# Optimization experiments

Hardware: AMD Instinct MI355X
Metric: run time of the kernel (lower is better)

Reference implementation:

```python
import jax, jax.numpy as jnp
import numpy as np

N_HEAD = 16
N_EMBD = 1024
SEQ = 2048
BATCH = 4


def setup_inputs() -> dict:
    key = jax.random.key(0)
    ks = jax.random.split(key, 5)
    s_in = 1.0 / np.sqrt(N_EMBD)
    return {
        "x": jax.random.normal(ks[0], (BATCH, SEQ, N_EMBD), dtype=jnp.float32),
        "W_attn": jax.random.normal(ks[1], (N_EMBD, 3 * N_EMBD), dtype=jnp.float32) * s_in,
        "b_attn": jax.random.normal(ks[2], (3 * N_EMBD,), dtype=jnp.float32) * 0.01,
        "W_proj": jax.random.normal(ks[3], (N_EMBD, N_EMBD), dtype=jnp.float32) * s_in,
        "b_proj": jax.random.normal(ks[4], (N_EMBD,), dtype=jnp.float32) * 0.01,
    }


def reference(x, W_attn, b_attn, W_proj, b_proj):
    B, T, C = x.shape
    H = N_HEAD
    D = C // H  # head dim
    qkv = x @ W_attn + b_attn                      # [B,T,3C]
    q, k, v = jnp.split(qkv, 3, axis=-1)
    # [B,T,C] -> [B,H,T,D]
    q = q.reshape(B, T, H, D).transpose(0, 2, 1, 3)
    k = k.reshape(B, T, H, D).transpose(0, 2, 1, 3)
    v = v.reshape(B, T, H, D).transpose(0, 2, 1, 3)
    scale = 1.0 / np.sqrt(D).astype(np.float32)
    att = jnp.einsum('bhqd,bhkd->bhqk', q, k) * scale   # [B,H,T,T]
    causal = jnp.tril(jnp.ones((T, T), dtype=bool))
    att = jnp.where(causal, att, jnp.finfo(att.dtype).min)
    att = jax.nn.softmax(att, axis=-1)
    y = jnp.einsum('bhqk,bhkd->bhqd', att, v)            # [B,H,T,D]
    y = y.transpose(0, 2, 1, 3).reshape(B, T, C)
    return y @ W_proj + b_proj
```

## Files before the change

### kernel.cpp

```cpp
#include <hip/hip_runtime.h>
#include <stdint.h>

typedef __attribute__((ext_vector_type(8))) short short8;
typedef __attribute__((ext_vector_type(4))) short short4v;
typedef __attribute__((ext_vector_type(4))) float f32x4;
typedef __attribute__((ext_vector_type(2))) unsigned int uint2v;

#define B_ 4
#define T_ 2048
#define C_ 1024
#define H_ 16
#define D_ 64
#define C3_ 3072

#define AS1 __attribute__((address_space(1)))
#define AS3 __attribute__((address_space(3)))

#define QK_SCALE 0.18033688f

__device__ __forceinline__ unsigned short f2bf(float f) {
    union { float f; uint32_t u; } v; v.f = f;
    uint32_t r = v.u + 0x7FFFu + ((v.u >> 16) & 1u);
    return (unsigned short)(r >> 16);
}

__device__ __forceinline__ uint32_t pk_bf16(float lo, float hi) {
    uint32_t r;
    asm("v_cvt_pk_bf16_f32 %0, %1, %2" : "=v"(r) : "v"(lo), "v"(hi));
    return r;
}

__global__ void k_cvt_bf16(const float* __restrict__ in, unsigned short* __restrict__ out, int n4) {
    int i = blockIdx.x * blockDim.x + threadIdx.x;
    if (i >= n4) return;
    float4 v = ((const float4*)in)[i];
    unsigned short o0 = f2bf(v.x), o1 = f2bf(v.y), o2 = f2bf(v.z), o3 = f2bf(v.w);
    unsigned long long packed = (unsigned long long)o0 | ((unsigned long long)o1 << 16)
        | ((unsigned long long)o2 << 32) | ((unsigned long long)o3 << 48);
    *(unsigned long long*)(out + (size_t)i * 4) = packed;
}

__global__ void k_wtrans(const float* __restrict__ W, unsigned short* __restrict__ WT, int K, int N) {
    __shared__ float t[32][33];
    int n0 = blockIdx.x * 32, k0 = blockIdx.y * 32;
    int tx = threadIdx.x, ty = threadIdx.y;
#pragma unroll
    for (int i = 0; i < 4; ++i)
        t[ty + i * 8][tx] = W[(size_t)(k0 + ty + i * 8) * N + n0 + tx];
    __syncthreads();
#pragma unroll
    for (int i = 0; i < 4; ++i)
        WT[(size_t)(n0 + ty + i * 8) * K + k0 + tx] = f2bf(t[tx][ty + i * 8]);
}

__global__ void k_prep_vt(const unsigned short* __restrict__ qkv, unsigned short* __restrict__ vt) {
    int bh = blockIdx.y; int b = bh >> 4, h = bh & 15;
    int t0 = blockIdx.x * 64;
    __shared__ unsigned short tile[64][72];
    int tid = threadIdx.x;
    int r = tid >> 3;
    int c = (tid & 7) * 8;
#pragma unroll
    for (int rr = 0; rr < 64; rr += 32) {
        const unsigned short* src = qkv + (size_t)(b * T_ + t0 + r + rr) * C3_ + 2 * C_ + h * D_ + c;
        short8 v = *(const short8*)src;
#pragma unroll
        for (int j = 0; j < 8; ++j) tile[r + rr][c + j] = (unsigned short)v[j];
    }
    __syncthreads();
#pragma unroll
    for (int rr = 0; rr < 64; rr += 32) {
        int d = r + rr;
        short8 sv;
#pragma unroll
        for (int j = 0; j < 8; ++j) sv[j] = (short)tile[c + j][d];
        *(short8*)(vt + (size_t)bh * D_ * T_ + (size_t)d * T_ + t0 + c) = sv;
    }
}

template<bool OUT_BF16>
__global__ __launch_bounds__(256, 2) void k_gemm_bt(const unsigned short* __restrict__ A,
                                                    const unsigned short* __restrict__ BT,
                                                    const float* __restrict__ bias,
                                                    unsigned short* __restrict__ outb,
                                                    float* __restrict__ outf,
                                                    int M, int N, int K) {
    __shared__ __align__(16) char arena[73728];
    int tid = threadIdx.x;
    int w = tid >> 6, lane = tid & 63;
    int wrow = w >> 1, wcol = w & 1;

    int lin = blockIdx.y * gridDim.x + blockIdx.x;
    int nwg8 = (gridDim.x * gridDim.y) >> 3;
    int newlin = (lin & 7) * nwg8 + (lin >> 3);
    int bx = newlin % gridDim.x;
    int by = newlin / gridDim.x;
    int m0 = by * 256, n0 = bx * 128;

    int lr = lane & 15, lg = lane >> 4;

    f32x4 acc[8][4] = {};

    int scb = ((tid & 3) << 4) ^ (((tid >> 3) & 3) << 4);
    int grow = tid >> 2;
    const char* sA[4];
    const char* sB[2];
#pragma unroll
    for (int rr = 0; rr < 4; ++rr)
        sA[rr] = (const char*)A + (size_t)(m0 + grow + rr * 64) * K * 2 + scb;
#pragma unroll
    for (int rr = 0; rr < 2; ++rr)
        sB[rr] = (const char*)BT + (size_t)(n0 + grow + rr * 64) * K * 2 + scb;

    int inner = (lg * 16) ^ (((lr >> 1) & 3) << 4);
    int aoff = wrow * 8192 + lr * 64 + inner;
    int boff = 16384 + wcol * 4096 + lr * 64 + inner;

#define GSTAGE(OFS)                                                                                 \
    {                                                                                               \
        _Pragma("unroll")                                                                           \
        for (int rr = 0; rr < 4; ++rr) {                                                            \
            __builtin_amdgcn_global_load_lds((const AS1 void*)sA[rr],                               \
                (AS3 void*)(arena + (OFS) + tid * 16 + rr * 4096), 16, 0, 0);                       \
            sA[rr] += 64;                                                                           \
        }                                                                                           \
        _Pragma("unroll")                                                                           \
        for (int rr = 0; rr < 2; ++rr) {                                                            \
            __builtin_amdgcn_global_load_lds((const AS1 void*)sB[rr],                               \
                (AS3 void*)(arena + (OFS) + 16384 + tid * 16 + rr * 4096), 16, 0, 0);               \
            sB[rr] += 64;                                                                           \
        }                                                                                           \
    }

#define GCOMPUTE(OFS)                                                                               \
    {                                                                                               \
        short8 af[8], bf[4];                                                                        \
        _Pragma("unroll")                                                                           \
        for (int i = 0; i < 8; ++i)                                                                 \
            af[i] = *(const short8*)(arena + (OFS) + aoff + i * 1024);                              \
        _Pragma("unroll")                                                                           \
        for (int j = 0; j < 4; ++j)                                                                 \
            bf[j] = *(const short8*)(arena + (OFS) + boff + j * 1024);                              \
        __builtin_amdgcn_s_setprio(1);                                                              \
        _Pragma("unroll")                                                                           \
        for (int i = 0; i < 8; ++i)                                                                 \
            _Pragma("unroll")                                                                       \
            for (int j = 0; j < 4; ++j)                                                             \
                acc[i][j] = __builtin_amdgcn_mfma_f32_16x16x32_bf16(af[i], bf[j], acc[i][j], 0, 0, 0); \
        __builtin_amdgcn_s_setprio(0);                                                              \
    }

    int NT = K >> 5;
    int ofs0 = 0, ofs1 = 24576, ofs2 = 49152;

    GSTAGE(ofs0);
    GSTAGE(ofs1);
    asm volatile("s_waitcnt vmcnt(6)" ::: "memory");
    __builtin_amdgcn_s_barrier();
    __builtin_amdgcn_sched_barrier(0);

    for (int t = 0; t < NT; ++t) {
        bool pf = (t + 2 < NT);
        if (pf) GSTAGE(ofs2);
        GCOMPUTE(ofs0);
        if (pf) { asm volatile("s_waitcnt vmcnt(6)" ::: "memory"); }
        else    { asm volatile("s_waitcnt vmcnt(0)" ::: "memory"); }
        __builtin_amdgcn_s_barrier();
        __builtin_amdgcn_sched_barrier(0);
        int tmp = ofs0; ofs0 = ofs1; ofs1 = ofs2; ofs2 = tmp;
    }
#undef GSTAGE
#undef GCOMPUTE

#pragma unroll
    for (int i = 0; i < 8; ++i) {
        int row = m0 + wrow * 128 + i * 16 + lg * 4;
#pragma unroll
        for (int j = 0; j < 4; ++j) {
            int col = n0 + wcol * 64 + j * 16 + lr;
            float bv = bias[col];
#pragma unroll
            for (int r = 0; r < 4; ++r) {
                float v = acc[i][j][r] + bv;
                if (OUT_BF16) {
                    if (col < C_) v *= QK_SCALE;
                    outb[(size_t)(row + r) * N + col] = f2bf(v);
                } else {
                    outf[(size_t)(row + r) * N + col] = v;
                }
            }
        }
    }
}

__global__ __launch_bounds__(256, 3) void k_gemm_bt128(const unsigned short* __restrict__ A,
                                                       const unsigned short* __restrict__ BT,
                                                       const float* __restrict__ bias,
                                                       float* __restrict__ outf,
                                                       int M, int N, int K) {
    __shared__ __align__(16) char arena[49152];
    int tid = threadIdx.x;
    int w = tid >> 6, lane = tid & 63;
    int wrow = w >> 1, wcol = w & 1;

    int lin = blockIdx.y * gridDim.x + blockIdx.x;
    int nwg8 = (gridDim.x * gridDim.y) >> 3;
    int newlin = (lin & 7) * nwg8 + (lin >> 3);
    int bx = newlin % gridDim.x;
    int by = newlin / gridDim.x;
    int m0 = by * 128, n0 = bx * 128;

    int lr = lane & 15, lg = lane >> 4;

    f32x4 acc[4][4] = {};

    int scb = ((tid & 3) << 4) ^ (((tid >> 3) & 3) << 4);
    int grow = tid >> 2;
    const char* sA[2];
    const char* sB[2];
#pragma unroll
    for (int rr = 0; rr < 2; ++rr) {
        sA[rr] = (const char*)A + (size_t)(m0 + grow + rr * 64) * K * 2 + scb;
        sB[rr] = (const char*)BT + (size_t)(n0 + grow + rr * 64) * K * 2 + scb;
    }

    int inner = (lg * 16) ^ (((lr >> 1) & 3) << 4);
    int aoff = wrow * 4096 + lr * 64 + inner;
    int boff = 8192 + wcol * 4096 + lr * 64 + inner;

#define GSTAGE(OFS)                                                                                 \
    {                                                                                               \
        _Pragma("unroll")                                                                           \
        for (int rr = 0; rr < 2; ++rr) {                                                            \
            __builtin_amdgcn_global_load_lds((const AS1 void*)sA[rr],                               \
                (AS3 void*)(arena + (OFS) + tid * 16 + rr * 4096), 16, 0, 0);                       \
            sA[rr] += 64;                                                                           \
            __builtin_amdgcn_global_load_lds((const AS1 void*)sB[rr],                               \
                (AS3 void*)(arena + (OFS) + 8192 + tid * 16 + rr * 4096), 16, 0, 0);                \
            sB[rr] += 64;                                                                           \
        }                                                                                           \
    }

#define GCOMPUTE(OFS)                                                                               \
    {                                                                                               \
        short8 af[4], bf[4];                                                                        \
        _Pragma("unroll")                                                                           \
        for (int i = 0; i < 4; ++i)                                                                 \
            af[i] = *(const short8*)(arena + (OFS) + aoff + i * 1024);                              \
        _Pragma("unroll")                                                                           \
        for (int j = 0; j < 4; ++j)                                                                 \
            bf[j] = *(const short8*)(arena + (OFS) + boff + j * 1024);                              \
        __builtin_amdgcn_s_setprio(1);                                                              \
        _Pragma("unroll")                                                                           \
        for (int i = 0; i < 4; ++i)                                                                 \
            _Pragma("unroll")                                                                       \
            for (int j = 0; j < 4; ++j)                                                             \
                acc[i][j] = __builtin_amdgcn_mfma_f32_16x16x32_bf16(af[i], bf[j], acc[i][j], 0, 0, 0); \
        __builtin_amdgcn_s_setprio(0);                                                              \
    }

    int NT = K >> 5;
    int ofs0 = 0, ofs1 = 16384, ofs2 = 32768;

    GSTAGE(ofs0);
    GSTAGE(ofs1);
    asm volatile("s_waitcnt vmcnt(4)" ::: "memory");
    __builtin_amdgcn_s_barrier();
    __builtin_amdgcn_sched_barrier(0);

    for (int t = 0; t < NT; ++t) {
        bool pf = (t + 2 < NT);
        if (pf) GSTAGE(ofs2);
        GCOMPUTE(ofs0);
        if (pf) { asm volatile("s_waitcnt vmcnt(4)" ::: "memory"); }
        else    { asm volatile("s_waitcnt vmcnt(0)" ::: "memory"); }
        __builtin_amdgcn_s_barrier();
        __builtin_amdgcn_sched_barrier(0);
        int tmp = ofs0; ofs0 = ofs1; ofs1 = ofs2; ofs2 = tmp;
    }
#undef GSTAGE
#undef GCOMPUTE

#pragma unroll
    for (int i = 0; i < 4; ++i) {
        int row = m0 + wrow * 64 + i * 16 + lg * 4;
#pragma unroll
        for (int j = 0; j < 4; ++j) {
            int col = n0 + wcol * 64 + j * 16 + lr;
            float bv = bias[col];
#pragma unroll
            for (int r = 0; r < 4; ++r)
                outf[(size_t)(row + r) * N + col] = acc[i][j][r] + bv;
        }
    }
}

__global__ __launch_bounds__(256, 4) void k_attn(const unsigned short* __restrict__ qkv,
                                                 const unsigned short* __restrict__ vt,
                                                 unsigned short* __restrict__ y) {
    __shared__ __align__(16) char arena[40960];
    int tid = threadIdx.x;
    int w = tid >> 6, lane = tid & 63;
    int lr = lane & 15, lg = lane >> 4;

    int bid = blockIdx.x;
    int bid2 = (bid & 7) * 128 + (bid >> 3);
    int bh = bid2 >> 4, pair = bid2 & 15;
    int b = bh >> 4, h = bh & 15;

    const unsigned short* kbase = qkv + (size_t)(b * T_) * C3_ + C_ + h * D_;
    const unsigned short* vtb = vt + (size_t)bh * D_ * T_;

    int sw_ = (lr & 7) << 4;
    int RB0 = lr * 128 + ((lg * 16) ^ sw_);
    int RB1 = RB0 ^ 64;
    int jl = (lr >> 1) & 3;
    int pbase = 32768 + w * 2048 + lr * 128
              + ((((lg >> 1) ^ (lr & 1)) << 4) | (((lg & 1) ^ (lr >> 3)) << 3));
    int pwa[4];
#pragma unroll
    for (int j = 0; j < 4; ++j) pwa[j] = pbase + ((j ^ jl) << 5);
    int prd0 = 32768 + w * 2048 + lr * 128 + ((lg ^ (lr & 7)) << 4);
    int prd1 = prd0 ^ 64;
    int hs = lr & 8;
    int prA0a = prd0 + hs,       prA0b = prd0 + (8 ^ hs);
    int prA1a = prd1 + hs,       prA1b = prd1 + (8 ^ hs);

    int row0 = tid >> 3, row1 = 32 + (tid >> 3);
    int scol0 = ((tid & 7) << 4) ^ ((row0 & 7) << 4);
    int scol1 = ((tid & 7) << 4) ^ ((row1 & 7) << 4);

    const char *sK0, *sK1, *sV0, *sV1;

#define ASTAGE(LDSOFF)                                                                                  \
    {                                                                                                   \
        __builtin_amdgcn_global_load_lds((const AS1 void*)sK0, (AS3 void*)(arena + (LDSOFF) + w * 1024), 16, 0, 0);          \
        __builtin_amdgcn_global_load_lds((const AS1 void*)sK1, (AS3 void*)(arena + (LDSOFF) + 4096 + w * 1024), 16, 0, 0);   \
        __builtin_amdgcn_global_load_lds((const AS1 void*)sV0, (AS3 void*)(arena + 16384 + (LDSOFF) + w * 1024), 16, 0, 0);  \
        __builtin_amdgcn_global_load_lds((const AS1 void*)sV1, (AS3 void*)(arena + 16384 + (LDSOFF) + 4096 + w * 1024), 16, 0, 0); \
        sK0 += 64 * C3_ * 2; sK1 += 64 * C3_ * 2; sV0 += 128; sV1 += 128;                               \
    }

#define ACOMPUTE(LDSOFF, KT)                                                                            \
    {                                                                                                   \
        f32x4 s[4];                                                                                     \
        __builtin_amdgcn_s_setprio(1);                                                                  \
        _Pragma("unroll")                                                                               \
        for (int j = 0; j < 4; ++j) {                                                                   \
            short8 kf0 = *(const short8*)(arena + RB0 + (LDSOFF) + j * 2048);                           \
            short8 kf1 = *(const short8*)(arena + RB1 + (LDSOFF) + j * 2048);                           \
            f32x4 z = {};                                                                               \
            z = __builtin_amdgcn_mfma_f32_16x16x32_bf16(kf0, qf0, z, 0, 0, 0);                          \
            s[j] = __builtin_amdgcn_mfma_f32_16x16x32_bf16(kf1, qf1, z, 0, 0, 0);                       \
        }                                                                                               \
        __builtin_amdgcn_s_setprio(0);                                                                  \
        if ((KT) == ntiles - 1) {                                                                       \
            int kb = (KT) * 64 + lg * 4 - qv;                                                           \
            _Pragma("unroll")                                                                           \
            for (int j = 0; j < 4; ++j)                                                                 \
                _Pragma("unroll")                                                                       \
                for (int r = 0; r < 4; ++r)                                                             \
                    if (kb + j * 16 + r > 0) s[j][r] = -INFINITY;                                       \
        }                                                                                               \
        _Pragma("unroll")                                                                               \
        for (int j = 0; j < 4; ++j)                                                                     \
            _Pragma("unroll")                                                                           \
            for (int r = 0; r < 4; ++r) {                                                               \
                float pv = __builtin_amdgcn_exp2f(s[j][r]);                                             \
                s[j][r] = pv;                                                                           \
                ls += pv;                                                                               \
            }                                                                                           \
        _Pragma("unroll")                                                                               \
        for (int j = 0; j < 4; ++j) {                                                                   \
            uint2v W;                                                                                   \
            W[0] = pk_bf16(s[j][0], s[j][1]);                                                           \
            W[1] = pk_bf16(s[j][2], s[j][3]);                                                           \
            *(uint2v*)(arena + pwa[j]) = W;                                                             \
        }                                                                                               \
        short4v l0 = *(const short4v*)(arena + prA0a);                                                  \
        short4v h0 = *(const short4v*)(arena + prA0b);                                                  \
        short4v l1 = *(const short4v*)(arena + prA1a);                                                  \
        short4v h1 = *(const short4v*)(arena + prA1b);                                                  \
        short8 pa0 = __builtin_shufflevector(l0, h0, 0, 1, 2, 3, 4, 5, 6, 7);                           \
        short8 pa1 = __builtin_shufflevector(l1, h1, 0, 1, 2, 3, 4, 5, 6, 7);                           \
        __builtin_amdgcn_s_setprio(1);                                                                  \
        _Pragma("unroll")                                                                               \
        for (int dt = 0; dt < 4; ++dt) {                                                                \
            short8 vf0 = *(const short8*)(arena + RB0 + 16384 + (LDSOFF) + dt * 2048);                  \
            short8 vf1 = *(const short8*)(arena + RB1 + 16384 + (LDSOFF) + dt * 2048);                  \
            o[dt] = __builtin_amdgcn_mfma_f32_16x16x32_bf16(pa0, vf0, o[dt], 0, 0, 0);                  \
            o[dt] = __builtin_amdgcn_mfma_f32_16x16x32_bf16(pa1, vf1, o[dt], 0, 0, 0);                  \
        }                                                                                               \
        __builtin_amdgcn_s_setprio(0);                                                                  \
    }

#pragma unroll 1
    for (int half = 0; half < 2; ++half) {
        int qt = half ? (31 - pair) : pair;
        int q0 = qt * 64;
        int ntiles = qt + 1;

        const unsigned short* qrow = qkv + (size_t)(b * T_ + q0 + w * 16 + lr) * C3_ + h * D_;
        short8 qf0 = *(const short8*)(qrow + lg * 8);
        short8 qf1 = *(const short8*)(qrow + 32 + lg * 8);

        f32x4 o[4] = {};
        float ls = 0.f;
        int qv = q0 + w * 16 + lr;

        sK0 = (const char*)(kbase + (size_t)row0 * C3_) + scol0;
        sK1 = (const char*)(kbase + (size_t)row1 * C3_) + scol1;
        sV0 = (const char*)(vtb + (size_t)row0 * T_) + scol0;
        sV1 = (const char*)(vtb + (size_t)row1 * T_) + scol1;

        ASTAGE(0);
        asm volatile("s_waitcnt vmcnt(0)" ::: "memory");
        __syncthreads();

#pragma unroll 1
        for (int kt = 0; kt < ntiles; kt += 2) {
            if (kt + 1 < ntiles) ASTAGE(8192);
            ACOMPUTE(0, kt);
            asm volatile("s_waitcnt vmcnt(0)" ::: "memory");
            __syncthreads();
            if (kt + 1 < ntiles) {
                if (kt + 2 < ntiles) ASTAGE(0);
                ACOMPUTE(8192, kt + 1);
                asm volatile("s_waitcnt vmcnt(0)" ::: "memory");
                __syncthreads();
            }
        }

        ls += __shfl_xor(ls, 16);
        ls += __shfl_xor(ls, 32);
#pragma unroll
        for (int r = 0; r < 4; ++r) {
            float lst = __shfl(ls, lg * 4 + r, 64);
            float inv = 1.0f / lst;
            int q = q0 + w * 16 + lg * 4 + r;
            unsigned short* yrow = y + (size_t)(b * T_ + q) * C_ + h * D_;
#pragma unroll
            for (int dt = 0; dt < 4; ++dt)
                yrow[dt * 16 + lr] = f2bf(o[dt][r] * inv);
        }
    }
#undef ASTAGE
#undef ACOMPUTE
}

extern "C" void kernel_launch(void* const* d_in, const int* in_sizes, int n_in,
                              void* d_out, int out_size, void* d_ws, size_t ws_size,
                              hipStream_t stream) {
    const float* x  = (const float*)d_in[0];
    const float* Wa = (const float*)d_in[1];
    const float* ba = (const float*)d_in[2];
    const float* Wp = (const float*)d_in[3];
    const float* bp = (const float*)d_in[4];
    float* out = (float*)d_out;

    char* ws = (char*)d_ws;
    unsigned short* xb  = (unsigned short*)(ws);
    unsigned short* wat = (unsigned short*)(ws + 16777216);
    unsigned short* wpt = (unsigned short*)(ws + 23068672);
    unsigned short* qkv = (unsigned short*)(ws + 25165824);
    unsigned short* vt  = (unsigned short*)(ws + 75497472);
    unsigned short* y   = xb;

    k_cvt_bf16<<<8192, 256, 0, stream>>>(x, xb, (B_ * T_ * C_) / 4);
    k_wtrans<<<dim3(C3_ / 32, C_ / 32), dim3(32, 8), 0, stream>>>(Wa, wat, C_, C3_);
    k_wtrans<<<dim3(C_ / 32, C_ / 32), dim3(32, 8), 0, stream>>>(Wp, wpt, C_, C_);
    k_gemm_bt<true><<<dim3(C3_ / 128, (B_ * T_) / 256), 256, 0, stream>>>(
        xb, wat, ba, qkv, nullptr, B_ * T_, C3_, C_);
    k_prep_vt<<<dim3(T_ / 64, B_ * H_), 256, 0, stream>>>(qkv, vt);
    k_attn<<<1024, 256, 0, stream>>>(qkv, vt, y);
    k_gemm_bt128<<<dim3(C_ / 128, (B_ * T_) / 128), 256, 0, stream>>>(
        y, wpt, bp, out, B_ * T_, C_, C_);
}
```

Measured before the change: 158.8 us.

## Double attention query tile per block to reuse K/V tiles across two row groups

Each wave in the attention kernel now handles 32 query rows (two 16-row groups) instead of 16, so every block covers a 128-row query tile. Each K/V tile staged into LDS therefore feeds twice as many MFMAs, and half as many blocks are launched. The P scratch area per wave doubles, so LDS grows to 48KB and the launch bound drops to 3 blocks per CU. Register pressure rises and fewer blocks are in flight. Causal masking is now applied over the last two key tiles to cover the larger diagonal.

```diff
diff --git a/kernel.cpp b/kernel.cpp
--- a/kernel.cpp
+++ b/kernel.cpp
@@ -295,17 +295,17 @@
     }
 }
 
-__global__ __launch_bounds__(256, 4) void k_attn(const unsigned short* __restrict__ qkv,
+__global__ __launch_bounds__(256, 3) void k_attn(const unsigned short* __restrict__ qkv,
                                                  const unsigned short* __restrict__ vt,
                                                  unsigned short* __restrict__ y) {
-    __shared__ __align__(16) char arena[40960];
+    __shared__ __align__(16) char arena[49152];
     int tid = threadIdx.x;
     int w = tid >> 6, lane = tid & 63;
     int lr = lane & 15, lg = lane >> 4;
 
     int bid = blockIdx.x;
-    int bid2 = (bid & 7) * 128 + (bid >> 3);
-    int bh = bid2 >> 4, pair = bid2 & 15;
+    int bid2 = (bid & 7) * 64 + (bid >> 3);
+    int bh = bid2 >> 3, pair = bid2 & 7;
     int b = bh >> 4, h = bh & 15;
 
     const unsigned short* kbase = qkv + (size_t)(b * T_) * C3_ + C_ + h * D_;
@@ -314,17 +314,18 @@
     int sw_ = (lr & 7) << 4;
     int RB0 = lr * 128 + ((lg * 16) ^ sw_);
     int RB1 = RB0 ^ 64;
+
     int jl = (lr >> 1) & 3;
-    int pbase = 32768 + w * 2048 + lr * 128
+    int pbase = 32768 + w * 4096 + lr * 128
               + ((((lg >> 1) ^ (lr & 1)) << 4) | (((lg & 1) ^ (lr >> 3)) << 3));
     int pwa[4];
 #pragma unroll
     for (int j = 0; j < 4; ++j) pwa[j] = pbase + ((j ^ jl) << 5);
-    int prd0 = 32768 + w * 2048 + lr * 128 + ((lg ^ (lr & 7)) << 4);
+    int prd0 = 32768 + w * 4096 + lr * 128 + ((lg ^ (lr & 7)) << 4);
     int prd1 = prd0 ^ 64;
     int hs = lr & 8;
-    int prA0a = prd0 + hs,       prA0b = prd0 + (8 ^ hs);
-    int prA1a = prd1 + hs,       prA1b = prd1 + (8 ^ hs);
+    int prA0a = prd0 + hs, prA0b = prd0 + (8 ^ hs);
+    int prA1a = prd1 + hs, prA1b = prd1 + (8 ^ hs);
 
     int row0 = tid >> 3, row1 = 32 + (tid >> 3);
     int scol0 = ((tid & 7) << 4) ^ ((row0 & 7) << 4);
@@ -343,70 +344,89 @@
 
 #define ACOMPUTE(LDSOFF, KT)                                                                            \
     {                                                                                                   \
-        f32x4 s[4];                                                                                     \
+        f32x4 s0[4], s1[4];                                                                             \
         __builtin_amdgcn_s_setprio(1);                                                                  \
         _Pragma("unroll")                                                                               \
         for (int j = 0; j < 4; ++j) {                                                                   \
             short8 kf0 = *(const short8*)(arena + RB0 + (LDSOFF) + j * 2048);                           \
             short8 kf1 = *(const short8*)(arena + RB1 + (LDSOFF) + j * 2048);                           \
-            f32x4 z = {};                                                                               \
-            z = __builtin_amdgcn_mfma_f32_16x16x32_bf16(kf0, qf0, z, 0, 0, 0);                          \
-            s[j] = __builtin_amdgcn_mfma_f32_16x16x32_bf16(kf1, qf1, z, 0, 0, 0);                       \
+            f32x4 z0 = {}, z1 = {};                                                                     \
+            z0 = __builtin_amdgcn_mfma_f32_16x16x32_bf16(kf0, qA0, z0, 0, 0, 0);                        \
+            s0[j] = __builtin_amdgcn_mfma_f32_16x16x32_bf16(kf1, qA1, z0, 0, 0, 0);                     \
+            z1 = __builtin_amdgcn_mfma_f32_16x16x32_bf16(kf0, qB0, z1, 0, 0, 0);                        \
+            s1[j] = __builtin_amdgcn_mfma_f32_16x16x32_bf16(kf1, qB1, z1, 0, 0, 0);                     \
         }                                                                                               \
         __builtin_amdgcn_s_setprio(0);                                                                  \
-        if ((KT) == ntiles - 1) {                                                                       \
-            int kb = (KT) * 64 + lg * 4 - qv;                                                           \
+        if ((KT) >= ntiles - 2) {                                                                       \
+            int kb0 = (KT) * 64 + lg * 4 - qv0;                                                         \
             _Pragma("unroll")                                                                           \
             for (int j = 0; j < 4; ++j)                                                                 \
                 _Pragma("unroll")                                                                       \
-                for (int r = 0; r < 4; ++r)                                                             \
-                    if (kb + j * 16 + r > 0) s[j][r] = -INFINITY;                                       \
+                for (int r = 0; r < 4; ++r) {                                                           \
+                    if (kb0 + j * 16 + r > 0)      s0[j][r] = -INFINITY;                                \
+                    if (kb0 - 16 + j * 16 + r > 0) s1[j][r] = -INFINITY;         \
+                }                                                                                       \
         }                                                                                               \
         _Pragma("unroll")                                                                               \
         for (int j = 0; j < 4; ++j)                                                                     \
             _Pragma("unroll")                                                                           \
             for (int r = 0; r < 4; ++r) {                                                               \
-                float pv = __builtin_amdgcn_exp2f(s[j][r]);                                             \
-                s[j][r] = pv;                                                                           \
-                ls += pv;                                                                               \
+                float p0 = __builtin_amdgcn_exp2f(s0[j][r]);                                            \
+                float p1 = __builtin_amdgcn_exp2f(s1[j][r]);                                            \
+                s0[j][r] = p0; ls0 += p0;                                                               \
+                s1[j][r] = p1; ls1 += p1;                                                               \
             }                                                                                           \
         _Pragma("unroll")                                                                               \
         for (int j = 0; j < 4; ++j) {                                                                   \
-            uint2v W;                                                                                   \
-            W[0] = pk_bf16(s[j][0], s[j][1]);                                                           \
-            W[1] = pk_bf16(s[j][2], s[j][3]);                                                           \
-            *(uint2v*)(arena + pwa[j]) = W;                                                             \
+            uint2v W0, W1;                                                                              \
+            W0[0] = pk_bf16(s0[j][0], s0[j][1]);                                                        \
+            W0[1] = pk_bf16(s0[j][2], s0[j][3]);                                                        \
+            W1[0] = pk_bf16(s1[j][0], s1[j][1]);                                                        \
+            W1[1] = pk_bf16(s1[j][2], s1[j][3]);                                                        \
+            *(uint2v*)(arena + pwa[j]) = W0;                                                            \
+            *(uint2v*)(arena + pwa[j] + 2048) = W1;                                                     \
         }                                                                                               \
-        short4v l0 = *(const short4v*)(arena + prA0a);                                                  \
-        short4v h0 = *(const short4v*)(arena + prA0b);                                                  \
-        short4v l1 = *(const short4v*)(arena + prA1a);                                                  \
-        short4v h1 = *(const short4v*)(arena + prA1b);                                                  \
-        short8 pa0 = __builtin_shufflevector(l0, h0, 0, 1, 2, 3, 4, 5, 6, 7);                           \
-        short8 pa1 = __builtin_shufflevector(l1, h1, 0, 1, 2, 3, 4, 5, 6, 7);                           \
+        short4v l00 = *(const short4v*)(arena + prA0a);                                                 \
+        short4v h00 = *(const short4v*)(arena + prA0b);                                                 \
+        short4v l01 = *(const short4v*)(arena + prA1a);                                                 \
+        short4v h01 = *(const short4v*)(arena + prA1b);                                                 \
+        short4v l10 = *(const short4v*)(arena + prA0a + 2048);                                          \
+        short4v h10 = *(const short4v*)(arena + prA0b + 2048);                                          \
+        short4v l11 = *(const short4v*)(arena + prA1a + 2048);                                          \
+        short4v h11 = *(const short4v*)(arena + prA1b + 2048);                                          \
+        short8 pa00 = __builtin_shufflevector(l00, h00, 0, 1, 2, 3, 4, 5, 6, 7);                        \
+        short8 pa01 = __builtin_shufflevector(l01, h01, 0, 1, 2, 3, 4, 5, 6, 7);                        \
+        short8 pa10 = __builtin_shufflevector(l10, h10, 0, 1, 2, 3, 4, 5, 6, 7);                        \
+        short8 pa11 = __builtin_shufflevector(l11, h11, 0, 1, 2, 3, 4, 5, 6, 7);                        \
         __builtin_amdgcn_s_setprio(1);                                                                  \
         _Pragma("unroll")                                                                               \
         for (int dt = 0; dt < 4; ++dt) {                                                                \
             short8 vf0 = *(const short8*)(arena + RB0 + 16384 + (LDSOFF) + dt * 2048);                  \
             short8 vf1 = *(const short8*)(arena + RB1 + 16384 + (LDSOFF) + dt * 2048);                  \
-            o[dt] = __builtin_amdgcn_mfma_f32_16x16x32_bf16(pa0, vf0, o[dt], 0, 0, 0);                  \
-            o[dt] = __builtin_amdgcn_mfma_f32_16x16x32_bf16(pa1, vf1, o[dt], 0, 0, 0);                  \
+            o0[dt] = __builtin_amdgcn_mfma_f32_16x16x32_bf16(pa00, vf0, o0[dt], 0, 0, 0);               \
+            o0[dt] = __builtin_amdgcn_mfma_f32_16x16x32_bf16(pa01, vf1, o0[dt], 0, 0, 0);               \
+            o1[dt] = __builtin_amdgcn_mfma_f32_16x16x32_bf16(pa10, vf0, o1[dt], 0, 0, 0);               \
+            o1[dt] = __builtin_amdgcn_mfma_f32_16x16x32_bf16(pa11, vf1, o1[dt], 0, 0, 0);               \
         }                                                                                               \
         __builtin_amdgcn_s_setprio(0);                                                                  \
     }
 
 #pragma unroll 1
     for (int half = 0; half < 2; ++half) {
-        int qt = half ? (31 - pair) : pair;
-        int q0 = qt * 64;
-        int ntiles = qt + 1;
-
-        const unsigned short* qrow = qkv + (size_t)(b * T_ + q0 + w * 16 + lr) * C3_ + h * D_;
-        short8 qf0 = *(const short8*)(qrow + lg * 8);
-        short8 qf1 = *(const short8*)(qrow + 32 + lg * 8);
-
-        f32x4 o[4] = {};
-        float ls = 0.f;
-        int qv = q0 + w * 16 + lr;
+        int qt = half ? (15 - pair) : pair;
+        int q0 = qt * 128;
+        int ntiles = 2 * qt + 2;
+
+        const unsigned short* qrowA = qkv + (size_t)(b * T_ + q0 + w * 32 + lr) * C3_ + h * D_;
+        const unsigned short* qrowB = qrowA + (size_t)16 * C3_;
+        short8 qA0 = *(const short8*)(qrowA + lg * 8);
+        short8 qA1 = *(const short8*)(qrowA + 32 + lg * 8);
+        short8 qB0 = *(const short8*)(qrowB + lg * 8);
+        short8 qB1 = *(const short8*)(qrowB + 32 + lg * 8);
+
+        f32x4 o0[4] = {}, o1[4] = {};
+        float ls0 = 0.f, ls1 = 0.f;
+        int qv0 = q0 + w * 32 + lr;
 
         sK0 = (const char*)(kbase + (size_t)row0 * C3_) + scol0;
         sK1 = (const char*)(kbase + (size_t)row1 * C3_) + scol1;
@@ -431,17 +451,21 @@
             }
         }
 
-        ls += __shfl_xor(ls, 16);
-        ls += __shfl_xor(ls, 32);
+        ls0 += __shfl_xor(ls0, 16); ls0 += __shfl_xor(ls0, 32);
+        ls1 += __shfl_xor(ls1, 16); ls1 += __shfl_xor(ls1, 32);
 #pragma unroll
         for (int r = 0; r < 4; ++r) {
-            float lst = __shfl(ls, lg * 4 + r, 64);
-            float inv = 1.0f / lst;
-            int q = q0 + w * 16 + lg * 4 + r;
-            unsigned short* yrow = y + (size_t)(b * T_ + q) * C_ + h * D_;
-#pragma unroll
-            for (int dt = 0; dt < 4; ++dt)
-                yrow[dt * 16 + lr] = f2bf(o[dt][r] * inv);
+            float l0 = __shfl(ls0, lg * 4 + r, 64);
+            float l1 = __shfl(ls1, lg * 4 + r, 64);
+            float i0 = 1.0f / l0, i1 = 1.0f / l1;
+            int qa = q0 + w * 32 + lg * 4 + r;
+            unsigned short* yrA = y + (size_t)(b * T_ + qa) * C_ + h * D_;
+            unsigned short* yrB = yrA + (size_t)16 * C_;
+#pragma unroll
+            for (int dt = 0; dt < 4; ++dt) {
+                yrA[dt * 16 + lr] = f2bf(o0[dt][r] * i0);
+                yrB[dt * 16 + lr] = f2bf(o1[dt][r] * i1);
+            }
         }
     }
 #undef ASTAGE
@@ -472,7 +496,7 @@
     k_gemm_bt<true><<<dim3(C3_ / 128, (B_ * T_) / 256), 256, 0, stream>>>(
         xb, wat, ba, qkv, nullptr, B_ * T_, C3_, C_);
     k_prep_vt<<<dim3(T_ / 64, B_ * H_), 256, 0, stream>>>(qkv, vt);
-    k_attn<<<1024, 256, 0, stream>>>(qkv, vt, y);
+    k_attn<<<512, 256, 0, stream>>>(qkv, vt, y);
     k_gemm_bt128<<<dim3(C_ / 128, (B_ * T_) / 128), 256, 0, stream>>>(
         y, wpt, bp, out, B_ * T_, C_, C_);
 }
```

New measurement: 158.5 us. About the same (-0.2%).

## Enlarge attention query tile to 128 rows with 8 waves; fuse prep kernels

Applied to the files above, without the earlier changes.

The attention kernel now runs 512-thread blocks covering 128 query rows, so each K/V tile staged into LDS is shared by twice as many waves. Each thread issues one K and one V load per stage, and the causal mask now covers the last two key tiles. The grid is halved and LDS per block grows. Separately, the x conversion and both weight-transpose kernels are merged into one launch to cut launch overhead. The risks are lower occupancy from the larger LDS and block size, and a more uneven causal workload per block.

```diff
diff --git a/kernel.cpp b/kernel.cpp
--- a/kernel.cpp
+++ b/kernel.cpp
@@ -30,20 +30,9 @@
     return r;
 }
 
-__global__ void k_cvt_bf16(const float* __restrict__ in, unsigned short* __restrict__ out, int n4) {
-    int i = blockIdx.x * blockDim.x + threadIdx.x;
-    if (i >= n4) return;
-    float4 v = ((const float4*)in)[i];
-    unsigned short o0 = f2bf(v.x), o1 = f2bf(v.y), o2 = f2bf(v.z), o3 = f2bf(v.w);
-    unsigned long long packed = (unsigned long long)o0 | ((unsigned long long)o1 << 16)
-        | ((unsigned long long)o2 << 32) | ((unsigned long long)o3 << 48);
-    *(unsigned long long*)(out + (size_t)i * 4) = packed;
-}
-
-__global__ void k_wtrans(const float* __restrict__ W, unsigned short* __restrict__ WT, int K, int N) {
-    __shared__ float t[32][33];
-    int n0 = blockIdx.x * 32, k0 = blockIdx.y * 32;
-    int tx = threadIdx.x, ty = threadIdx.y;
+__device__ __forceinline__ void wtrans_body(const float* __restrict__ W, unsigned short* __restrict__ WT,
+                                            int K, int N, int n0, int k0, int tx, int ty,
+                                            float (*t)[33]) {
 #pragma unroll
     for (int i = 0; i < 4; ++i)
         t[ty + i * 8][tx] = W[(size_t)(k0 + ty + i * 8) * N + n0 + tx];
@@ -51,6 +40,28 @@
 #pragma unroll
     for (int i = 0; i < 4; ++i)
         WT[(size_t)(n0 + ty + i * 8) * K + k0 + tx] = f2bf(t[tx][ty + i * 8]);
+}
+
+__global__ __launch_bounds__(256) void k_prep(const float* __restrict__ x, unsigned short* __restrict__ xb,
+                                              const float* __restrict__ Wa, unsigned short* __restrict__ wat,
+                                              const float* __restrict__ Wp, unsigned short* __restrict__ wpt) {
+    __shared__ float t[32][33];
+    int bid = blockIdx.x;
+    int tid = threadIdx.x;
+    if (bid < 8192) {
+        int i = bid * 256 + tid;
+        float4 v = ((const float4*)x)[i];
+        unsigned short o0 = f2bf(v.x), o1 = f2bf(v.y), o2 = f2bf(v.z), o3 = f2bf(v.w);
+        unsigned long long packed = (unsigned long long)o0 | ((unsigned long long)o1 << 16)
+            | ((unsigned long long)o2 << 32) | ((unsigned long long)o3 << 48);
+        *(unsigned long long*)(xb + (size_t)i * 4) = packed;
+    } else if (bid < 11264) {
+        int lb = bid - 8192;
+        wtrans_body(Wa, wat, C_, C3_, (lb % 96) * 32, (lb / 96) * 32, tid & 31, tid >> 5, t);
+    } else {
+        int lb = bid - 11264;
+        wtrans_body(Wp, wpt, C_, C_, (lb % 32) * 32, (lb / 32) * 32, tid & 31, tid >> 5, t);
+    }
 }
 
 __global__ void k_prep_vt(const unsigned short* __restrict__ qkv, unsigned short* __restrict__ vt) {
@@ -295,17 +306,17 @@
     }
 }
 
-__global__ __launch_bounds__(256, 4) void k_attn(const unsigned short* __restrict__ qkv,
+__global__ __launch_bounds__(512, 4) void k_attn(const unsigned short* __restrict__ qkv,
                                                  const unsigned short* __restrict__ vt,
                                                  unsigned short* __restrict__ y) {
-    __shared__ __align__(16) char arena[40960];
+    __shared__ __align__(16) char arena[49152];
     int tid = threadIdx.x;
     int w = tid >> 6, lane = tid & 63;
     int lr = lane & 15, lg = lane >> 4;
 
     int bid = blockIdx.x;
-    int bid2 = (bid & 7) * 128 + (bid >> 3);
-    int bh = bid2 >> 4, pair = bid2 & 15;
+    int bid2 = (bid & 7) * 64 + (bid >> 3);
+    int bh = bid2 >> 3, pair = bid2 & 7;
     int b = bh >> 4, h = bh & 15;
 
     const unsigned short* kbase = qkv + (size_t)(b * T_) * C3_ + C_ + h * D_;
@@ -314,6 +325,7 @@
     int sw_ = (lr & 7) << 4;
     int RB0 = lr * 128 + ((lg * 16) ^ sw_);
     int RB1 = RB0 ^ 64;
+
     int jl = (lr >> 1) & 3;
     int pbase = 32768 + w * 2048 + lr * 128
               + ((((lg >> 1) ^ (lr & 1)) << 4) | (((lg & 1) ^ (lr >> 3)) << 3));
@@ -323,22 +335,19 @@
     int prd0 = 32768 + w * 2048 + lr * 128 + ((lg ^ (lr & 7)) << 4);
     int prd1 = prd0 ^ 64;
     int hs = lr & 8;
-    int prA0a = prd0 + hs,       prA0b = prd0 + (8 ^ hs);
-    int prA1a = prd1 + hs,       prA1b = prd1 + (8 ^ hs);
-
-    int row0 = tid >> 3, row1 = 32 + (tid >> 3);
-    int scol0 = ((tid & 7) << 4) ^ ((row0 & 7) << 4);
-    int scol1 = ((tid & 7) << 4) ^ ((row1 & 7) << 4);
-
-    const char *sK0, *sK1, *sV0, *sV1;
+    int prA0a = prd0 + hs, prA0b = prd0 + (8 ^ hs);
+    int prA1a = prd1 + hs, prA1b = prd1 + (8 ^ hs);
+
+    int grow = tid >> 3;
+    int scol = ((tid & 7) << 4) ^ ((grow & 7) << 4);
+
+    const char *sK, *sV;
 
 #define ASTAGE(LDSOFF)                                                                                  \
     {                                                                                                   \
-        __builtin_amdgcn_global_load_lds((const AS1 void*)sK0, (AS3 void*)(arena + (LDSOFF) + w * 1024), 16, 0, 0);          \
-        __builtin_amdgcn_global_load_lds((const AS1 void*)sK1, (AS3 void*)(arena + (LDSOFF) + 4096 + w * 1024), 16, 0, 0);   \
-        __builtin_amdgcn_global_load_lds((const AS1 void*)sV0, (AS3 void*)(arena + 16384 + (LDSOFF) + w * 1024), 16, 0, 0);  \
-        __builtin_amdgcn_global_load_lds((const AS1 void*)sV1, (AS3 void*)(arena + 16384 + (LDSOFF) + 4096 + w * 1024), 16, 0, 0); \
-        sK0 += 64 * C3_ * 2; sK1 += 64 * C3_ * 2; sV0 += 128; sV1 += 128;                               \
+        __builtin_amdgcn_global_load_lds((const AS1 void*)sK, (AS3 void*)(arena + (LDSOFF) + tid * 16), 16, 0, 0);           \
+        __builtin_amdgcn_global_load_lds((const AS1 void*)sV, (AS3 void*)(arena + 16384 + (LDSOFF) + tid * 16), 16, 0, 0);   \
+        sK += 64 * C3_ * 2; sV += 128;                                                                  \
     }
 
 #define ACOMPUTE(LDSOFF, KT)                                                                            \
@@ -354,7 +363,7 @@
             s[j] = __builtin_amdgcn_mfma_f32_16x16x32_bf16(kf1, qf1, z, 0, 0, 0);                       \
         }                                                                                               \
         __builtin_amdgcn_s_setprio(0);                                                                  \
-        if ((KT) == ntiles - 1) {                                                                       \
+        if ((KT) >= ntiles - 2) {                                                                       \
             int kb = (KT) * 64 + lg * 4 - qv;                                                           \
             _Pragma("unroll")                                                                           \
             for (int j = 0; j < 4; ++j)                                                                 \
@@ -396,9 +405,9 @@
 
 #pragma unroll 1
     for (int half = 0; half < 2; ++half) {
-        int qt = half ? (31 - pair) : pair;
-        int q0 = qt * 64;
-        int ntiles = qt + 1;
+        int qt = half ? (15 - pair) : pair;
+        int q0 = qt * 128;
+        int ntiles = 2 * qt + 2;
 
         const unsigned short* qrow = qkv + (size_t)(b * T_ + q0 + w * 16 + lr) * C3_ + h * D_;
         short8 qf0 = *(const short8*)(qrow + lg * 8);
@@ -408,10 +417,8 @@
         float ls = 0.f;
         int qv = q0 + w * 16 + lr;
 
-        sK0 = (const char*)(kbase + (size_t)row0 * C3_) + scol0;
-        sK1 = (const char*)(kbase + (size_t)row1 * C3_) + scol1;
-        sV0 = (const char*)(vtb + (size_t)row0 * T_) + scol0;
-        sV1 = (const char*)(vtb + (size_t)row1 * T_) + scol1;
+        sK = (const char*)(kbase + (size_t)grow * C3_) + scol;
+        sV = (const char*)(vtb + (size_t)grow * T_) + scol;
 
         ASTAGE(0);
         asm volatile("s_waitcnt vmcnt(0)" ::: "memory");
@@ -466,13 +473,11 @@
     unsigned short* vt  = (unsigned short*)(ws + 75497472);
     unsigned short* y   = xb;
 
-    k_cvt_bf16<<<8192, 256, 0, stream>>>(x, xb, (B_ * T_ * C_) / 4);
-    k_wtrans<<<dim3(C3_ / 32, C_ / 32), dim3(32, 8), 0, stream>>>(Wa, wat, C_, C3_);
-    k_wtrans<<<dim3(C_ / 32, C_ / 32), dim3(32, 8), 0, stream>>>(Wp, wpt, C_, C_);
+    k_prep<<<12288, 256, 0, stream>>>(x, xb, Wa, wat, Wp, wpt);
     k_gemm_bt<true><<<dim3(C3_ / 128, (B_ * T_) / 256), 256, 0, stream>>>(
         xb, wat, ba, qkv, nullptr, B_ * T_, C3_, C_);
     k_prep_vt<<<dim3(T_ / 64, B_ * H_), 256, 0, stream>>>(qkv, vt);
-    k_attn<<<1024, 256, 0, stream>>>(qkv, vt, y);
+    k_attn<<<512, 512, 0, stream>>>(qkv, vt, y);
     k_gemm_bt128<<<dim3(C_ / 128, (B_ * T_) / 128), 256, 0, stream>>>(
         y, wpt, bp, out, B_ * T_, C_, C_);
 }
```

Result: faster. 151.5 us (-4.6%).
